# Performance work log

Hardware: AMD Instinct MI355X
Metric: run time of the kernel (lower is better)

Reference implementation:

```python
import jax, jax.numpy as jnp
import numpy as np

DIM = 768
HEADS = 8
HEAD_DIM = DIM // HEADS
SCALE = DIM ** (-0.5)  # faithful: original scales by dimension**-0.5, not head_dim


def setup_inputs() -> dict:
    key = jax.random.key(0)
    k1, k2, k3 = jax.random.split(key, 3)
    B, N = 2, 4096
    x = jax.random.normal(k1, (B, N, DIM), dtype=jnp.float32)
    # qkv projection params (Linear(dim, 3*dim))
    W_qkv = jax.random.normal(k2, (DIM, 3 * DIM), dtype=jnp.float32) * (DIM ** -0.5)
    b_qkv = jax.random.normal(k3, (3 * DIM,), dtype=jnp.float32) * 0.01
    return {"x": x, "W_qkv": W_qkv, "b_qkv": b_qkv}


def reference(x, W_qkv, b_qkv):
    B, N, D = x.shape
    qkv = x @ W_qkv + b_qkv                       # (B, N, 3D)
    qkv = qkv.reshape(B, N, 3, HEADS, HEAD_DIM)
    q, k, v = jnp.moveaxis(qkv, 2, 0)             # each (B, N, H, dh)
    # (B, H, N, N) scores — explicit materialization as in the source
    scores = jnp.einsum('bnhd,bmhd->bhnm', q, k) * SCALE
    attn = jax.nn.softmax(scores, axis=-1)
    out = jnp.einsum('bhnm,bmhd->bnhd', attn, v)  # (B, N, H, dh)
    return out.reshape(B, N, D)
```

## Files before the change

kernel.cpp:

```cpp
#include <hip/hip_runtime.h>
#include <hip/hip_bf16.h>


typedef __attribute__((ext_vector_type(8)))  short    bf16x8;
typedef __attribute__((ext_vector_type(4)))  float    floatx4;
typedef __attribute__((ext_vector_type(16))) float    floatx16;
typedef __attribute__((ext_vector_type(8)))  unsigned short us8;
typedef __attribute__((ext_vector_type(4)))  unsigned short us4;

#define HEADS 8
#define DH 96
#define NSEQ 4096
#define DIM 768
#define SCALE2_F (0.03608439182435161f * 1.4426950408889634f)

#define GLOAD16(g, s) __builtin_amdgcn_global_load_lds(                              \
    (const __attribute__((address_space(1))) unsigned int*)(g),                      \
    (__attribute__((address_space(3))) unsigned int*)(s), 16, 0, 0)

__device__ __forceinline__ unsigned short f2bf(float f) {
    union { float f; unsigned u; } v; v.f = f;
    unsigned r = v.u + 0x7fffu + ((v.u >> 16) & 1u);
    return (unsigned short)(r >> 16);
}

__device__ __forceinline__ unsigned pk2(float a, float b) {
    float2 t; t.x = a; t.y = b;
    __hip_bfloat162 r = __float22bfloat162_rn(t);
    return *(unsigned*)&r;
}

__device__ __forceinline__ bf16x8 mk_pfrag(float c0, float c1, float c2, float c3,
                                           float c4, float c5, float c6, float c7, int hB) {
    unsigned pl0 = pk2(c0, c1), pl1 = pk2(c2, c3);
    unsigned pu0 = pk2(c4, c5), pu1 = pk2(c6, c7);
    unsigned s0 = hB ? pl0 : pu0, s1 = hB ? pl1 : pu1;
    unsigned r0 = (unsigned)__shfl_xor((int)s0, 32);
    unsigned r1 = (unsigned)__shfl_xor((int)s1, 32);
    union { unsigned u[4]; bf16x8 v; } f;
    f.u[0] = hB ? r0 : pl0;
    f.u[1] = hB ? r1 : pl1;
    f.u[2] = hB ? pu0 : r0;
    f.u[3] = hB ? pu1 : r1;
    return f.v;
}

__global__ __launch_bounds__(256) void cvt_x(const float* __restrict__ x, unsigned short* __restrict__ xb) {
    int i = blockIdx.x * 256 + threadIdx.x;
    float4 v = ((const float4*)x)[i];
    us4 o; o.x = f2bf(v.x); o.y = f2bf(v.y); o.z = f2bf(v.z); o.w = f2bf(v.w);
    ((us4*)xb)[i] = o;
}

__global__ __launch_bounds__(256) void cvt_w(const float* __restrict__ w, unsigned short* __restrict__ wt) {
    __shared__ unsigned short sm[64][33];
    int c0 = blockIdx.x * 32, k0 = blockIdx.y * 64;
    int t = threadIdx.x;
    int cl = t & 31, kl0 = t >> 5;
    for (int i = 0; i < 8; ++i) {
        int kl = kl0 + i * 8;
        sm[kl][cl] = f2bf(w[(k0 + kl) * 2304 + c0 + cl]);
    }
    __syncthreads();
    int kl2 = t & 63, cl0 = t >> 6;
    for (int i = 0; i < 8; ++i) {
        int cl2 = cl0 + i * 4;
        wt[(c0 + cl2) * 768 + k0 + kl2] = sm[kl2][cl2];
    }
}

__global__ __launch_bounds__(256) void gemm_qkv(const unsigned short* __restrict__ xb,
                                                const unsigned short* __restrict__ wt,
                                                const float* __restrict__ bias,
                                                unsigned short* __restrict__ qb,
                                                unsigned short* __restrict__ kb,
                                                unsigned short* __restrict__ vt) {
    __shared__ unsigned short As[2][128 * 64];
    __shared__ unsigned short Bs[2][128 * 64];
    const int tid = threadIdx.x;
    const int lane = tid & 63, wv = tid >> 6;
    const int n15 = lane & 15, quad = lane >> 4;
    const int x7q = n15 & 7;
    const int mw = (wv >> 1) * 64, nw = (wv & 1) * 64;
    const int lrow = lane >> 3;
    const int lcolsw = ((lane & 7) ^ lrow) * 8;
    const int lofs = wv * 8 * 64;
    floatx4 acc[4][4] = {};

    const int raw = blockIdx.x;
    const int id = (raw & 7) * 144 + (raw >> 3);
    const bool isv = id >= 768;
    int m0, c0;
    const unsigned short *gA, *gB;
    if (!isv) {
        m0 = (id / 12) * 128; c0 = (id % 12) * 128;
        gA = xb + (size_t)(m0 + wv * 8 + lrow) * 768 + lcolsw;
        gB = wt + (size_t)(c0 + wv * 8 + lrow) * 768 + lcolsw;
    } else {
        int iv = id - 768;
        c0 = (iv / 6) * 128; m0 = (iv % 6) * 128;
        gA = wt + (size_t)(1536 + m0 + wv * 8 + lrow) * 768 + lcolsw;
        gB = xb + (size_t)(c0 + wv * 8 + lrow) * 768 + lcolsw;
    }

    auto stage = [&](int b, int kt) {
#pragma unroll
        for (int i = 0; i < 4; ++i) {
            GLOAD16(gA + (size_t)i * 32 * 768 + kt * 64, &As[b][lofs + i * 32 * 64]);
            GLOAD16(gB + (size_t)i * 32 * 768 + kt * 64, &Bs[b][lofs + i * 32 * 64]);
        }
    };

    stage(0, 0);
    __syncthreads();
#pragma unroll 2
    for (int kt = 0; kt < 12; ++kt) {
        const int cur = kt & 1;
        if (kt < 11) stage(cur ^ 1, kt + 1);
#pragma unroll
        for (int ks = 0; ks < 2; ++ks) {
            bf16x8 af[4], bfr[4];
            for (int mt = 0; mt < 4; ++mt)
                af[mt] = *(const bf16x8*)&As[cur][(mw + mt * 16 + n15) * 64
                                                 + (((ks << 2) + quad) ^ x7q) * 8];
            for (int nt = 0; nt < 4; ++nt)
                bfr[nt] = *(const bf16x8*)&Bs[cur][(nw + nt * 16 + n15) * 64
                                                  + (((ks << 2) + quad) ^ x7q) * 8];
            for (int mt = 0; mt < 4; ++mt)
                for (int nt = 0; nt < 4; ++nt)
                    acc[mt][nt] = __builtin_amdgcn_mfma_f32_16x16x32_bf16(af[mt], bfr[nt], acc[mt][nt], 0, 0, 0);
        }
        __syncthreads();
    }

    if (!isv) {
        for (int nt = 0; nt < 4; ++nt) {
            int c = c0 + nw + nt * 16 + n15;
            float bv = bias[c];
            int which = c / 768, rem = c % 768;
            int h = rem / 96, d = rem % 96;
            for (int mt = 0; mt < 4; ++mt) {
                for (int r = 0; r < 4; ++r) {
                    int m = m0 + mw + mt * 16 + quad * 4 + r;
                    int b = m >> 12, n = m & 4095;
                    float val = acc[mt][nt][r] + bv;
                    int bh = b * HEADS + h;
                    if (which == 0) qb[(bh * NSEQ + n) * DH + d] = f2bf(val * SCALE2_F);
                    else            kb[(bh * NSEQ + n) * DH + d] = f2bf(val);
                }
            }
        }
    } else {
        for (int mt = 0; mt < 4; ++mt) {
            for (int r = 0; r < 4; ++r) {
                int dv = m0 + mw + mt * 16 + quad * 4 + r;
                float bv = bias[1536 + dv];
                int h = dv / 96, d = dv % 96;
                for (int nt = 0; nt < 4; ++nt) {
                    int ng = c0 + nw + nt * 16 + n15;
                    int b = ng >> 12, n = ng & 4095;
                    vt[((size_t)(b * HEADS + h) * DH + d) * NSEQ + n] = f2bf(acc[mt][nt][r] + bv);
                }
            }
        }
    }
}

__global__ __launch_bounds__(256, 2) void flash(const unsigned short* __restrict__ qb,
                                                const unsigned short* __restrict__ kb,
                                                const unsigned short* __restrict__ vt,
                                                float* __restrict__ out) {
    __shared__ unsigned short sm[34816];
    __shared__ float l_all[128];

    const int tid = threadIdx.x;
    const int lane = tid & 63, wv = tid >> 6;
    const int l31 = lane & 31, h = lane >> 5;
    const int x7 = l31 & 7;
    const int id = blockIdx.x;
    const int bh = id & 15;
    const int q0 = (id >> 4) * 128 + wv * 32;

    const unsigned short* kgb = kb + (size_t)bh * NSEQ * DH;
    const unsigned short* vgb = vt + (size_t)bh * DH * NSEQ;

    bf16x8 qf[6];
    {
        const unsigned short* qrow = qb + (size_t)(bh * NSEQ + q0 + l31) * DH;
#pragma unroll
        for (int ks = 0; ks < 6; ++ks)
            qf[ks] = *(const bf16x8*)&qrow[ks * 16 + h * 8];
    }

    int kofs[2][6];
#pragma unroll
    for (int kt = 0; kt < 2; ++kt)
#pragma unroll
        for (int ks = 0; ks < 6; ++ks) {
            int b = 2 * ks + h;
            int bs = (b < 8) ? (b ^ x7) : (8 + ((b - 8) ^ x7));
            kofs[kt][ks] = (kt * 32 + l31) * 128 + bs * 8;
        }
    int vofs[3][4];
#pragma unroll
    for (int dt = 0; dt < 3; ++dt)
#pragma unroll
        for (int s = 0; s < 4; ++s)
            vofs[dt][s] = (dt * 32 + l31) * 64 + ((2 * s + h) ^ x7) * 8;

    int goffk[3], goffv[3], wofk[3], wofv[3];
#pragma unroll
    for (int i = 0; i < 3; ++i) {
        int tb = i * 256 + tid;
        int r = tb / 12, bb = tb % 12;
        goffk[i] = r * 96 + bb * 8;
        int bs = (bb < 8) ? (bb ^ (r & 7)) : (8 + ((bb - 8) ^ (r & 7)));
        wofk[i] = r * 128 + bs * 8;
        int d = tb >> 3, b2 = tb & 7;
        goffv[i] = d * 4096 + b2 * 8;
        wofv[i] = d * 64 + ((b2 ^ (d & 7))) * 8;
    }

    const floatx16 z16 = (floatx16)(0.f);

    us8 kr[3], vr[3];
    const unsigned short* kpf = kgb;
    const unsigned short* vpf = vgb;
#pragma unroll
    for (int i = 0; i < 3; ++i) { kr[i] = *(const us8*)&kpf[goffk[i]]; vr[i] = *(const us8*)&vpf[goffv[i]]; }
    kpf += 6144; vpf += 64;
#pragma unroll
    for (int i = 0; i < 3; ++i) { *(us8*)&sm[wofk[i]] = kr[i]; *(us8*)&sm[16384 + wofv[i]] = vr[i]; }
#pragma unroll
    for (int i = 0; i < 3; ++i) { kr[i] = *(const us8*)&kpf[goffk[i]]; vr[i] = *(const us8*)&vpf[goffv[i]]; }
    kpf += 6144; vpf += 64;
    __syncthreads();

    floatx16 stA[2], stB[2];
#pragma unroll
    for (int ks = 0; ks < 6; ++ks)
#pragma unroll
        for (int kt = 0; kt < 2; ++kt) {
            bf16x8 ak = *(const bf16x8*)&sm[kofs[kt][ks]];
            stA[kt] = __builtin_amdgcn_mfma_f32_32x32x16_bf16(ak, qf[ks], ks == 0 ? z16 : stA[kt], 0, 0, 0);
        }

    floatx16 o[3] = {};
    float lsum = 0.f;

    auto body = [&](int kv, floatx16 (&cur)[2], floatx16 (&nxt)[2]) {
        if (kv < 63) {
            unsigned short* Kd = sm + ((kv + 1) & 1) * 8192;
            unsigned short* Vd = sm + 16384 + ((kv + 1) % 3) * 6144;
#pragma unroll
            for (int i = 0; i < 3; ++i) { *(us8*)&Kd[wofk[i]] = kr[i]; *(us8*)&Vd[wofv[i]] = vr[i]; }
            if (kv < 62) {
#pragma unroll
                for (int i = 0; i < 3; ++i) { kr[i] = *(const us8*)&kpf[goffk[i]]; vr[i] = *(const us8*)&vpf[goffv[i]]; }
                kpf += 6144; vpf += 64;
            }
        }
        __syncthreads();

        if (kv < 63) {
            const unsigned short* Kn = sm + ((kv + 1) & 1) * 8192;
#pragma unroll
            for (int ks = 0; ks < 6; ++ks)
#pragma unroll
                for (int kt = 0; kt < 2; ++kt) {
                    bf16x8 ak = *(const bf16x8*)&Kn[kofs[kt][ks]];
                    nxt[kt] = __builtin_amdgcn_mfma_f32_32x32x16_bf16(ak, qf[ks], ks == 0 ? z16 : nxt[kt], 0, 0, 0);
                }
        }

#pragma unroll
        for (int kt = 0; kt < 2; ++kt)
#pragma unroll
            for (int rg = 0; rg < 16; ++rg) {
                float p = __builtin_amdgcn_exp2f(cur[kt][rg]);
                cur[kt][rg] = p;
                lsum += p;
            }
        bf16x8 pf[4];
        pf[0] = mk_pfrag(cur[0][0], cur[0][1], cur[0][2], cur[0][3],
                         cur[0][4], cur[0][5], cur[0][6], cur[0][7], h);
        pf[1] = mk_pfrag(cur[0][8], cur[0][9], cur[0][10], cur[0][11],
                         cur[0][12], cur[0][13], cur[0][14], cur[0][15], h);
        pf[2] = mk_pfrag(cur[1][0], cur[1][1], cur[1][2], cur[1][3],
                         cur[1][4], cur[1][5], cur[1][6], cur[1][7], h);
        pf[3] = mk_pfrag(cur[1][8], cur[1][9], cur[1][10], cur[1][11],
                         cur[1][12], cur[1][13], cur[1][14], cur[1][15], h);

        const unsigned short* Vc = sm + 16384 + (kv % 3) * 6144;
#pragma unroll
        for (int s = 0; s < 4; ++s)
#pragma unroll
            for (int dt = 0; dt < 3; ++dt) {
                bf16x8 bv = *(const bf16x8*)&Vc[vofs[dt][s]];
                o[dt] = __builtin_amdgcn_mfma_f32_32x32x16_bf16(pf[s], bv, o[dt], 0, 0, 0);
            }
    };

    for (int kv = 0; kv < 64; kv += 2) {
        body(kv, stA, stB);
        body(kv + 1, stB, stA);
    }

    lsum += __shfl_xor(lsum, 32);
    if (h == 0) l_all[wv * 32 + l31] = lsum;
    __syncthreads();

    const int b = bh >> 3, hd = bh & 7;
#pragma unroll
    for (int rg = 0; rg < 16; ++rg) {
        int row = (rg & 3) + 8 * (rg >> 2) + 4 * h;
        float inv = 1.0f / l_all[wv * 32 + row];
        int q = q0 + row;
        float* op = out + (size_t)(b * NSEQ + q) * DIM + hd * DH;
#pragma unroll
        for (int dt = 0; dt < 3; ++dt)
            op[dt * 32 + l31] = o[dt][rg] * inv;
    }
}

extern "C" void kernel_launch(void* const* d_in, const int* in_sizes, int n_in,
                              void* d_out, int out_size, void* d_ws, size_t ws_size,
                              hipStream_t stream) {
    const float* x    = (const float*)d_in[0];
    const float* W    = (const float*)d_in[1];
    const float* bias = (const float*)d_in[2];
    float* out = (float*)d_out;

    char* ws = (char*)d_ws;
    unsigned short* xb = (unsigned short*)(ws);
    unsigned short* wt = (unsigned short*)(ws + 12582912);
    unsigned short* qb = (unsigned short*)(ws + 16121856);
    unsigned short* kb = (unsigned short*)(ws + 28704768);
    unsigned short* vt = (unsigned short*)(ws + 41287680);

    cvt_x<<<6144, 256, 0, stream>>>(x, xb);
    cvt_w<<<dim3(72, 12), 256, 0, stream>>>(W, wt);
    gemm_qkv<<<1152, 256, 0, stream>>>(xb, wt, bias, qb, kb, vt);
    flash<<<512, 256, 0, stream>>>(qb, kb, vt, out);
}
```

Baseline: 250.8 us.

## Split flash attention over KV halves with a combine pass; merge conversion kernels

The flash kernel now optionally splits the key/value sequence into two halves, launching twice as many blocks. Each block writes unnormalised partial outputs and row sums to workspace, and a new combine kernel adds the halves and normalises. The split relies on the lack of max subtraction, so partial exp sums combine without rescaling. It also fuses the x and W bf16 conversion kernels into one launch. The split path adds about 50 MB of extra fp32 partial writes and reads plus one more launch, and it runs only when the workspace is large enough.

```diff
diff --git a/kernel.cpp b/kernel.cpp
--- a/kernel.cpp
+++ b/kernel.cpp
@@ -45,27 +45,32 @@
     return f.v;
 }
 
-__global__ __launch_bounds__(256) void cvt_x(const float* __restrict__ x, unsigned short* __restrict__ xb) {
-    int i = blockIdx.x * 256 + threadIdx.x;
-    float4 v = ((const float4*)x)[i];
-    us4 o; o.x = f2bf(v.x); o.y = f2bf(v.y); o.z = f2bf(v.z); o.w = f2bf(v.w);
-    ((us4*)xb)[i] = o;
-}
-
-__global__ __launch_bounds__(256) void cvt_w(const float* __restrict__ w, unsigned short* __restrict__ wt) {
+__global__ __launch_bounds__(256) void cvt(const float* __restrict__ x,
+                                           const float* __restrict__ w,
+                                           unsigned short* __restrict__ xb,
+                                           unsigned short* __restrict__ wt) {
     __shared__ unsigned short sm[64][33];
-    int c0 = blockIdx.x * 32, k0 = blockIdx.y * 64;
-    int t = threadIdx.x;
-    int cl = t & 31, kl0 = t >> 5;
-    for (int i = 0; i < 8; ++i) {
-        int kl = kl0 + i * 8;
-        sm[kl][cl] = f2bf(w[(k0 + kl) * 2304 + c0 + cl]);
-    }
-    __syncthreads();
-    int kl2 = t & 63, cl0 = t >> 6;
-    for (int i = 0; i < 8; ++i) {
-        int cl2 = cl0 + i * 4;
-        wt[(c0 + cl2) * 768 + k0 + kl2] = sm[kl2][cl2];
+    const int bid = blockIdx.x;
+    const int t = threadIdx.x;
+    if (bid < 6144) {
+        int i = bid * 256 + t;
+        float4 v = ((const float4*)x)[i];
+        us4 o; o.x = f2bf(v.x); o.y = f2bf(v.y); o.z = f2bf(v.z); o.w = f2bf(v.w);
+        ((us4*)xb)[i] = o;
+    } else {
+        int wb = bid - 6144;
+        int c0 = (wb % 72) * 32, k0 = (wb / 72) * 64;
+        int cl = t & 31, kl0 = t >> 5;
+        for (int i = 0; i < 8; ++i) {
+            int kl = kl0 + i * 8;
+            sm[kl][cl] = f2bf(w[(k0 + kl) * 2304 + c0 + cl]);
+        }
+        __syncthreads();
+        int kl2 = t & 63, cl0 = t >> 6;
+        for (int i = 0; i < 8; ++i) {
+            int cl2 = cl0 + i * 4;
+            wt[(c0 + cl2) * 768 + k0 + kl2] = sm[kl2][cl2];
+        }
     }
 }
 
@@ -166,10 +171,12 @@
     }
 }
 
+template<int SPLIT>
 __global__ __launch_bounds__(256, 2) void flash(const unsigned short* __restrict__ qb,
                                                 const unsigned short* __restrict__ kb,
                                                 const unsigned short* __restrict__ vt,
-                                                float* __restrict__ out) {
+                                                float* __restrict__ outp,
+                                                float* __restrict__ lp) {
     __shared__ unsigned short sm[34816];
     __shared__ float l_all[128];
 
@@ -177,12 +184,15 @@
     const int lane = tid & 63, wv = tid >> 6;
     const int l31 = lane & 31, h = lane >> 5;
     const int x7 = l31 & 7;
-    const int id = blockIdx.x;
+    const int idg = blockIdx.x;
+    const int half = SPLIT ? (idg >> 9) : 0;
+    const int id = SPLIT ? (idg & 511) : idg;
     const int bh = id & 15;
     const int q0 = (id >> 4) * 128 + wv * 32;
-
-    const unsigned short* kgb = kb + (size_t)bh * NSEQ * DH;
-    const unsigned short* vgb = vt + (size_t)bh * DH * NSEQ;
+    const int NT = SPLIT ? 32 : 64;
+
+    const unsigned short* kgb = kb + (size_t)bh * NSEQ * DH + (size_t)half * 2048 * DH;
+    const unsigned short* vgb = vt + (size_t)bh * DH * NSEQ + (size_t)half * 2048;
 
     bf16x8 qf[6];
     {
@@ -249,12 +259,12 @@
     float lsum = 0.f;
 
     auto body = [&](int kv, floatx16 (&cur)[2], floatx16 (&nxt)[2]) {
-        if (kv < 63) {
+        if (kv < NT - 1) {
             unsigned short* Kd = sm + ((kv + 1) & 1) * 8192;
             unsigned short* Vd = sm + 16384 + ((kv + 1) % 3) * 6144;
 #pragma unroll
             for (int i = 0; i < 3; ++i) { *(us8*)&Kd[wofk[i]] = kr[i]; *(us8*)&Vd[wofv[i]] = vr[i]; }
-            if (kv < 62) {
+            if (kv < NT - 2) {
 #pragma unroll
                 for (int i = 0; i < 3; ++i) { kr[i] = *(const us8*)&kpf[goffk[i]]; vr[i] = *(const us8*)&vpf[goffv[i]]; }
                 kpf += 6144; vpf += 64;
@@ -262,7 +272,7 @@
         }
         __syncthreads();
 
-        if (kv < 63) {
+        if (kv < NT - 1) {
             const unsigned short* Kn = sm + ((kv + 1) & 1) * 8192;
 #pragma unroll
             for (int ks = 0; ks < 6; ++ks)
@@ -301,26 +311,60 @@
             }
     };
 
-    for (int kv = 0; kv < 64; kv += 2) {
+    for (int kv = 0; kv < NT; kv += 2) {
         body(kv, stA, stB);
         body(kv + 1, stB, stA);
     }
 
     lsum += __shfl_xor(lsum, 32);
-    if (h == 0) l_all[wv * 32 + l31] = lsum;
-    __syncthreads();
-
     const int b = bh >> 3, hd = bh & 7;
-#pragma unroll
-    for (int rg = 0; rg < 16; ++rg) {
-        int row = (rg & 3) + 8 * (rg >> 2) + 4 * h;
-        float inv = 1.0f / l_all[wv * 32 + row];
-        int q = q0 + row;
-        float* op = out + (size_t)(b * NSEQ + q) * DIM + hd * DH;
-#pragma unroll
-        for (int dt = 0; dt < 3; ++dt)
-            op[dt * 32 + l31] = o[dt][rg] * inv;
-    }
+
+    if (SPLIT) {
+        if (h == 0) lp[(size_t)(half * 16 + bh) * NSEQ + q0 + l31] = lsum;
+        float* ob = outp + (size_t)half * (2 * NSEQ * DIM);
+#pragma unroll
+        for (int rg = 0; rg < 16; ++rg) {
+            int row = (rg & 3) + 8 * (rg >> 2) + 4 * h;
+            int q = q0 + row;
+            float* op = ob + (size_t)(b * NSEQ + q) * DIM + hd * DH;
+#pragma unroll
+            for (int dt = 0; dt < 3; ++dt)
+                op[dt * 32 + l31] = o[dt][rg];
+        }
+    } else {
+        if (h == 0) l_all[wv * 32 + l31] = lsum;
+        __syncthreads();
+#pragma unroll
+        for (int rg = 0; rg < 16; ++rg) {
+            int row = (rg & 3) + 8 * (rg >> 2) + 4 * h;
+            float inv = 1.0f / l_all[wv * 32 + row];
+            int q = q0 + row;
+            float* op = outp + (size_t)(b * NSEQ + q) * DIM + hd * DH;
+#pragma unroll
+            for (int dt = 0; dt < 3; ++dt)
+                op[dt * 32 + l31] = o[dt][rg] * inv;
+        }
+    }
+}
+
+__global__ __launch_bounds__(256) void combine(const float* __restrict__ P,
+                                               const float* __restrict__ ls,
+                                               float* __restrict__ out) {
+    int i = blockIdx.x * 256 + threadIdx.x;
+    int row = i / 192;
+    int hd = (i % 192) / 24;
+    int b = row >> 12, q = row & 4095;
+    int bh = b * HEADS + hd;
+    float l = ls[bh * NSEQ + q] + ls[16 * NSEQ + bh * NSEQ + q];
+    float inv = 1.0f / l;
+    float4 v0 = ((const float4*)P)[i];
+    float4 v1 = ((const float4*)P)[1572864 + i];
+    float4 r;
+    r.x = (v0.x + v1.x) * inv;
+    r.y = (v0.y + v1.y) * inv;
+    r.z = (v0.z + v1.z) * inv;
+    r.w = (v0.w + v1.w) * inv;
+    ((float4*)out)[i] = r;
 }
 
 extern "C" void kernel_launch(void* const* d_in, const int* in_sizes, int n_in,
@@ -337,9 +381,16 @@
     unsigned short* qb = (unsigned short*)(ws + 16121856);
     unsigned short* kb = (unsigned short*)(ws + 28704768);
     unsigned short* vt = (unsigned short*)(ws + 41287680);
-
-    cvt_x<<<6144, 256, 0, stream>>>(x, xb);
-    cvt_w<<<dim3(72, 12), 256, 0, stream>>>(W, wt);
+    float* Opart = (float*)(ws + 53870592);
+    float* lpart = (float*)(ws + 104202240);
+    const size_t WS_NEED = 104726528;
+
+    cvt<<<7008, 256, 0, stream>>>(x, W, xb, wt);
     gemm_qkv<<<1152, 256, 0, stream>>>(xb, wt, bias, qb, kb, vt);
-    flash<<<512, 256, 0, stream>>>(qb, kb, vt, out);
-}
+    if (ws_size >= WS_NEED) {
+        flash<1><<<1024, 256, 0, stream>>>(qb, kb, vt, Opart, lpart);
+        combine<<<6144, 256, 0, stream>>>(Opart, lpart, out);
+    } else {
+        flash<0><<<512, 256, 0, stream>>>(qb, kb, vt, out, nullptr);
+    }
+}
```

After: 263.9 us. 1.05x slower.
